# Kernel optimization log

Hardware: AMD Instinct MI355X
Metric: run time of the kernel (lower is better)

The kernel has to match this reference:

```python
import jax, jax.numpy as jnp
import numpy as np

EMBED_DIM = 768
NUM_HEADS = 12
HEAD_DIM = EMBED_DIM // NUM_HEADS


def setup_inputs() -> dict:
    key = jax.random.key(0)
    ks = jax.random.split(key, 12)
    B, T, D, Hp, Wp = 4, 32, EMBED_DIM, 16, 16
    h = jax.random.normal(ks[0], (B, T, D, Hp, Wp), dtype=jnp.float32)
    u_enc = jax.random.uniform(ks[1], (B, T, D, Hp, Wp), dtype=jnp.float32)
    lam = jax.random.uniform(ks[2], (B, T, 1, Hp, Wp), dtype=jnp.float32)
    s = 1.0 / np.sqrt(D)
    Wq = jax.random.normal(ks[3], (D, D), dtype=jnp.float32) * s
    bq = jnp.zeros((D,), dtype=jnp.float32)
    Wk = jax.random.normal(ks[4], (D, D), dtype=jnp.float32) * s
    bk = jnp.zeros((D,), dtype=jnp.float32)
    Wv = jax.random.normal(ks[5], (D, D), dtype=jnp.float32) * s
    bv = jnp.zeros((D,), dtype=jnp.float32)
    Wo = jax.random.normal(ks[6], (D, D), dtype=jnp.float32) * s
    bo = jnp.zeros((D,), dtype=jnp.float32)
    return {"h": h, "u_enc": u_enc, "lam": lam,
            "Wq": Wq, "bq": bq, "Wk": Wk, "bk": bk,
            "Wv": Wv, "bv": bv, "Wo": Wo, "bo": bo}


def reference(h, u_enc, lam, Wq, bq, Wk, bk, Wv, bv, Wo, bo):
    B, T, D, Hp, Wp = h.shape
    S = Hp * Wp
    NH, HD = NUM_HEADS, HEAD_DIM
    # (B,T,D,Hp,Wp) -> (B*S, T, D)
    h_seq = jnp.transpose(h, (0, 3, 4, 1, 2)).reshape(B * S, T, D)
    u_seq = jnp.transpose(u_enc, (0, 3, 4, 1, 2)).reshape(B * S, T, D)
    lam_seq = jnp.transpose(lam, (0, 3, 4, 1, 2)).reshape(B * S, T)
    # projections (nn.Linear: x @ W.T + b)
    Q = (h_seq @ Wq.T + bq).reshape(B * S, T, NH, HD).transpose(0, 2, 1, 3)
    K = (h_seq @ Wk.T + bk).reshape(B * S, T, NH, HD).transpose(0, 2, 1, 3)
    V = (h_seq @ Wv.T + bv).reshape(B * S, T, NH, HD).transpose(0, 2, 1, 3)
    scores = jnp.einsum('bhqd,bhkd->bhqk', Q, K) / jnp.sqrt(jnp.float32(HD))
    # key-dependent uncertainty penalty: lam_j * mean_d(u_j)
    u_pen = lam_seq * u_seq.mean(axis=-1)  # (B*S, T)
    scores = scores - u_pen[:, None, None, :]
    attn = jax.nn.softmax(scores, axis=-1)  # dropout: eval mode (identity)
    out = jnp.einsum('bhqk,bhkd->bhqd', attn, V)
    out = out.transpose(0, 2, 1, 3).reshape(B * S, T, D)
    out = out @ Wo.T + bo
    return jnp.transpose(out.reshape(B, Hp, Wp, T, D), (0, 3, 4, 1, 2))
```

## Files before the change

kernel.cpp:

```cpp
#include <hip/hip_runtime.h>

typedef float   f32x4 __attribute__((ext_vector_type(4)));
typedef _Float16 f16x8 __attribute__((ext_vector_type(8)));

#define DEV static __device__ __forceinline__

#define BB 4
#define TT 32
#define DD 768
#define SS 256
#define NHD 12
#define HD 64
#define NSEQ  (BB*SS)
#define MTOK  (NSEQ*TT)

DEV void async_copy16(const _Float16* g, _Float16* l) {
  __builtin_amdgcn_global_load_lds(
      (const __attribute__((address_space(1))) unsigned int*)g,
      (__attribute__((address_space(3))) unsigned int*)l,
      16, 0, 0);
}

DEV int swz_chunk(int r, int kc) {
  return r * 4 + (kc ^ (r & 3) ^ ((r >> 2) & 3));
}

__global__ __launch_bounds__(256) void k_transpose_h(const float* __restrict__ h,
                                                     _Float16* __restrict__ A) {
  __shared__ _Float16 Tl[256 * 65];
  const int slab = blockIdx.x;
  const int d0   = blockIdx.y * 64;
  const int t    = threadIdx.x;
  const float4* hv = (const float4*)(h + (slab * DD + d0) * SS);
  #pragma unroll
  for (int i = 0; i < 16; ++i) {
    int dd = i * 4 + (t >> 6);
    int s4 = (t & 63) * 4;
    float4 v = hv[dd * 64 + (t & 63)];
    Tl[(s4 + 0) * 65 + dd] = (_Float16)v.x;
    Tl[(s4 + 1) * 65 + dd] = (_Float16)v.y;
    Tl[(s4 + 2) * 65 + dd] = (_Float16)v.z;
    Tl[(s4 + 3) * 65 + dd] = (_Float16)v.w;
  }
  __syncthreads();
  #pragma unroll
  for (int p = 0; p < 8; ++p) {
    int s  = p * 32 + (t >> 3);
    int dd = (t & 7) * 8;
    f16x8 val;
    #pragma unroll
    for (int j = 0; j < 8; ++j) val[j] = Tl[s * 65 + dd + j];
    *(f16x8*)(A + (slab * SS + s) * DD + d0 + dd) = val;
  }
}

__global__ __launch_bounds__(256) void k_convert_w(const float* __restrict__ Wq,
                                                   const float* __restrict__ Wk,
                                                   const float* __restrict__ Wv,
                                                   const float* __restrict__ Wo,
                                                   _Float16* __restrict__ WQKV,
                                                   _Float16* __restrict__ WoH) {
  int idx = blockIdx.x * 256 + threadIdx.x;
  int row = idx / 96;
  int c8  = (idx % 96) * 8;
  const float* src; _Float16* dst;
  if (row < 768)       { src = Wq + row * 768;          dst = WQKV + row * 768; }
  else if (row < 1536) { src = Wk + (row - 768) * 768;  dst = WQKV + row * 768; }
  else if (row < 2304) { src = Wv + (row - 1536) * 768; dst = WQKV + row * 768; }
  else                 { src = Wo + (row - 2304) * 768; dst = WoH  + (row - 2304) * 768; }
  float4 v0 = *(const float4*)(src + c8);
  float4 v1 = *(const float4*)(src + c8 + 4);
  f16x8 o;
  o[0]=(_Float16)v0.x; o[1]=(_Float16)v0.y; o[2]=(_Float16)v0.z; o[3]=(_Float16)v0.w;
  o[4]=(_Float16)v1.x; o[5]=(_Float16)v1.y; o[6]=(_Float16)v1.z; o[7]=(_Float16)v1.w;
  *(f16x8*)(dst + c8) = o;
}

__global__ __launch_bounds__(256) void k_upen(const float* __restrict__ u,
                                              const float* __restrict__ lam,
                                              float* __restrict__ upen) {
  int slab = blockIdx.x >> 2;
  int q    = blockIdx.x & 3;
  int s    = threadIdx.x;
  const float* base = u + (slab * DD + q * 192) * SS + s;
  float sum = 0.f;
  for (int d = 0; d < 192; ++d) sum += base[d * SS];
  int b = slab >> 5, tt = slab & 31;
  float l = lam[slab * SS + s];
  atomicAdd(&upen[(b * SS + s) * TT + tt], sum * l * (1.0f / 768.0f));
}

__global__ __launch_bounds__(256, 2) void k_gemm_qkv(const _Float16* __restrict__ A,
                                                     const _Float16* __restrict__ Bw,
                                                     const float* __restrict__ bq,
                                                     const float* __restrict__ bk,
                                                     const float* __restrict__ bv,
                                                     _Float16* __restrict__ Qp,
                                                     _Float16* __restrict__ Kp,
                                                     _Float16* __restrict__ Vp) {
  __shared__ _Float16 As[128 * 32];
  __shared__ _Float16 Bs[256 * 32];
  const int mt = blockIdx.x & 255, nt = blockIdx.x >> 8;
  const int m0 = mt * 128, n0 = nt * 256;
  const int tid = threadIdx.x, w = tid >> 6, lane = tid & 63;
  const int wr = (w >> 1) * 64, wcc = (w & 1) * 128;
  f32x4 acc[4][8] = {};
  for (int it = 0; it < 24; ++it) {
    const int k0 = it * 32;
    __syncthreads();
    #pragma unroll
    for (int i = 0; i < 2; ++i) {
      int c = tid + 256 * i;
      int row = c >> 2;
      int coff = ((c & 3) ^ (row & 3) ^ ((row >> 2) & 3)) * 8;
      _Float16* ldsA = (_Float16*)((char*)As + (w * 1024 + i * 4096 + lane * 16));
      async_copy16(A + (m0 + row) * DD + k0 + coff, ldsA);
    }
    #pragma unroll
    for (int i = 0; i < 4; ++i) {
      int c = tid + 256 * i;
      int row = c >> 2;
      int coff = ((c & 3) ^ (row & 3) ^ ((row >> 2) & 3)) * 8;
      _Float16* ldsB = (_Float16*)((char*)Bs + (w * 1024 + i * 4096 + lane * 16));
      async_copy16(Bw + (n0 + row) * DD + k0 + coff, ldsB);
    }
    __syncthreads();
    f16x8 af[4], bf[8];
    #pragma unroll
    for (int mi = 0; mi < 4; ++mi)
      af[mi] = *(const f16x8*)&As[swz_chunk(wr + mi * 16 + (lane & 15), lane >> 4) * 8];
    #pragma unroll
    for (int ni = 0; ni < 8; ++ni)
      bf[ni] = *(const f16x8*)&Bs[swz_chunk(wcc + ni * 16 + (lane & 15), lane >> 4) * 8];
    #pragma unroll
    for (int mi = 0; mi < 4; ++mi)
      #pragma unroll
      for (int ni = 0; ni < 8; ++ni)
        acc[mi][ni] = __builtin_amdgcn_mfma_f32_16x16x32_f16(af[mi], bf[ni], acc[mi][ni], 0, 0, 0);
  }
  const int sel = nt / 3;
  const float scale = (sel == 0) ? 0.125f : 1.0f;
  const float* bias = (sel == 0) ? bq : ((sel == 1) ? bk : bv);
  _Float16* dst = (sel == 0) ? Qp : ((sel == 1) ? Kp : Vp);
  const int slab = mt >> 1, s0 = (mt & 1) * 128;
  const int b = slab >> 5, t = slab & 31;
  #pragma unroll
  for (int ni = 0; ni < 8; ++ni) {
    int n768 = nt * 256 - sel * 768 + wcc + ni * 16 + (lane & 15);
    int head = n768 >> 6, hd = n768 & 63;
    float bs = bias[n768];
    long hb = (long)head * 2048 + t * 64 + hd;
    #pragma unroll
    for (int mi = 0; mi < 4; ++mi) {
      f32x4 v = acc[mi][ni];
      #pragma unroll
      for (int r = 0; r < 4; ++r) {
        int s = s0 + wr + mi * 16 + (lane >> 4) * 4 + r;
        long seq = b * 256 + s;
        dst[seq * 24576 + hb] = (_Float16)((v[r] + bs) * scale);
      }
    }
  }
}

__global__ __launch_bounds__(256) void k_attn(const _Float16* __restrict__ Qp,
                                              const _Float16* __restrict__ Kp,
                                              const _Float16* __restrict__ Vp,
                                              const float* __restrict__ upen,
                                              _Float16* __restrict__ O) {
  __shared__ _Float16 lds[4][32 * 66 + 32 * 40];
  const int w = threadIdx.x >> 6, lane = threadIdx.x & 63;
  const int seq = blockIdx.x / 3, hg = blockIdx.x % 3;
  const int head = hg * 4 + w;
  const int b = seq >> 8, s = seq & 255;
  _Float16* Vs = &lds[w][0];
  _Float16* Ps = &lds[w][32 * 66];
  const long base = (long)(seq * NHD + head) * 2048;
  const _Float16* Qb = Qp + base;
  const _Float16* Kb = Kp + base;
  const _Float16* Vb = Vp + base;

  {
    int t = lane & 31, hh = (lane >> 5) * 32;
    f16x8 vc[4];
    #pragma unroll
    for (int c = 0; c < 4; ++c) vc[c] = *(const f16x8*)(Vb + t * 64 + hh + c * 8);
    #pragma unroll
    for (int c = 0; c < 4; ++c)
      #pragma unroll
      for (int p = 0; p < 4; ++p) {
        union { _Float16 h[2]; unsigned u; } pk;
        pk.h[0] = vc[c][2 * p]; pk.h[1] = vc[c][2 * p + 1];
        *(unsigned*)&Vs[t * 66 + hh + c * 8 + 2 * p] = pk.u;
      }
  }
  f16x8 qf[2][2], kf[2][2];
  #pragma unroll
  for (int i = 0; i < 2; ++i)
    #pragma unroll
    for (int ks = 0; ks < 2; ++ks) {
      int off = (i * 16 + (lane & 15)) * 64 + ks * 32 + (lane >> 4) * 8;
      qf[i][ks] = *(const f16x8*)(Qb + off);
      kf[i][ks] = *(const f16x8*)(Kb + off);
    }
  f32x4 sc[2][2] = {};
  #pragma unroll
  for (int mq = 0; mq < 2; ++mq)
    #pragma unroll
    for (int nk = 0; nk < 2; ++nk)
      #pragma unroll
      for (int ks = 0; ks < 2; ++ks)
        sc[mq][nk] = __builtin_amdgcn_mfma_f32_16x16x32_f16(qf[mq][ks], kf[nk][ks], sc[mq][nk], 0, 0, 0);

  const float up0 = upen[seq * TT + (lane & 15)];
  const float up1 = upen[seq * TT + 16 + (lane & 15)];

  #pragma unroll
  for (int mq = 0; mq < 2; ++mq) {
    #pragma unroll
    for (int r = 0; r < 4; ++r) {
      float s0 = sc[mq][0][r] - up0;
      float s1 = sc[mq][1][r] - up1;
      float mx = fmaxf(s0, s1);
      #pragma unroll
      for (int off = 1; off < 16; off <<= 1) mx = fmaxf(mx, __shfl_xor(mx, off, 64));
      float e0 = __expf(s0 - mx), e1 = __expf(s1 - mx);
      float sum = e0 + e1;
      #pragma unroll
      for (int off = 1; off < 16; off <<= 1) sum += __shfl_xor(sum, off, 64);
      float inv = 1.0f / sum;
      int row = mq * 16 + (lane >> 4) * 4 + r;
      Ps[row * 40 + (lane & 15)]      = (_Float16)(e0 * inv);
      Ps[row * 40 + 16 + (lane & 15)] = (_Float16)(e1 * inv);
    }
  }
  f16x8 pf[2];
  #pragma unroll
  for (int mq = 0; mq < 2; ++mq)
    pf[mq] = *(const f16x8*)(Ps + (mq * 16 + (lane & 15)) * 40 + (lane >> 4) * 8);
  f32x4 oacc[2][4] = {};
  #pragma unroll
  for (int nh = 0; nh < 4; ++nh) {
    int hd = nh * 16 + (lane & 15);
    f16x8 vf;
    #pragma unroll
    for (int j = 0; j < 8; ++j) vf[j] = Vs[((lane >> 4) * 8 + j) * 66 + hd];
    #pragma unroll
    for (int mq = 0; mq < 2; ++mq)
      oacc[mq][nh] = __builtin_amdgcn_mfma_f32_16x16x32_f16(pf[mq], vf, oacc[mq][nh], 0, 0, 0);
  }
  #pragma unroll
  for (int mq = 0; mq < 2; ++mq)
    #pragma unroll
    for (int nh = 0; nh < 4; ++nh) {
      int hd = nh * 16 + (lane & 15);
      #pragma unroll
      for (int r = 0; r < 4; ++r) {
        int t = mq * 16 + (lane >> 4) * 4 + r;
        O[((long)((b << 5) + t) * SS + s) * DD + head * HD + hd] = (_Float16)oacc[mq][nh][r];
      }
    }
}

__global__ __launch_bounds__(256, 2) void k_gemm_out(const _Float16* __restrict__ Wn,
                                                     const _Float16* __restrict__ O,
                                                     const float* __restrict__ bo,
                                                     float* __restrict__ out) {
  __shared__ _Float16 As[128 * 32];
  __shared__ _Float16 Bs[256 * 32];
  const int ct = blockIdx.x & 127, rt = blockIdx.x >> 7;
  const int R0 = rt * 128, C0 = ct * 256;
  const int tid = threadIdx.x, w = tid >> 6, lane = tid & 63;
  const int wr = (w >> 1) * 64, wcc = (w & 1) * 128;
  f32x4 acc[4][8] = {};
  for (int it = 0; it < 24; ++it) {
    const int k0 = it * 32;
    __syncthreads();
    #pragma unroll
    for (int i = 0; i < 2; ++i) {
      int c = tid + 256 * i;
      int row = c >> 2;
      int coff = ((c & 3) ^ (row & 3) ^ ((row >> 2) & 3)) * 8;
      _Float16* ldsA = (_Float16*)((char*)As + (w * 1024 + i * 4096 + lane * 16));
      async_copy16(Wn + (R0 + row) * DD + k0 + coff, ldsA);
    }
    #pragma unroll
    for (int i = 0; i < 4; ++i) {
      int c = tid + 256 * i;
      int row = c >> 2;
      int coff = ((c & 3) ^ (row & 3) ^ ((row >> 2) & 3)) * 8;
      _Float16* ldsB = (_Float16*)((char*)Bs + (w * 1024 + i * 4096 + lane * 16));
      async_copy16(O + (C0 + row) * DD + k0 + coff, ldsB);
    }
    __syncthreads();
    f16x8 af[4], bf[8];
    #pragma unroll
    for (int ri = 0; ri < 4; ++ri)
      af[ri] = *(const f16x8*)&As[swz_chunk(wr + ri * 16 + (lane & 15), lane >> 4) * 8];
    #pragma unroll
    for (int ci = 0; ci < 8; ++ci)
      bf[ci] = *(const f16x8*)&Bs[swz_chunk(wcc + ci * 16 + (lane & 15), lane >> 4) * 8];
    #pragma unroll
    for (int ri = 0; ri < 4; ++ri)
      #pragma unroll
      for (int ci = 0; ci < 8; ++ci)
        acc[ri][ci] = __builtin_amdgcn_mfma_f32_16x16x32_f16(af[ri], bf[ci], acc[ri][ci], 0, 0, 0);
  }
  const int slab = ct;
  #pragma unroll
  for (int ri = 0; ri < 4; ++ri) {
    #pragma unroll
    for (int ci = 0; ci < 8; ++ci) {
      int s = wcc + ci * 16 + (lane & 15);
      f32x4 v = acc[ri][ci];
      #pragma unroll
      for (int r = 0; r < 4; ++r) {
        int R = R0 + wr + ri * 16 + (lane >> 4) * 4 + r;
        out[((long)slab * DD + R) * SS + s] = v[r] + bo[R];
      }
    }
  }
}

extern "C" void kernel_launch(void* const* d_in, const int* in_sizes, int n_in,
                              void* d_out, int out_size, void* d_ws, size_t ws_size,
                              hipStream_t stream) {
  const float* h   = (const float*)d_in[0];
  const float* u   = (const float*)d_in[1];
  const float* lam = (const float*)d_in[2];
  const float* Wq  = (const float*)d_in[3];
  const float* bq  = (const float*)d_in[4];
  const float* Wk  = (const float*)d_in[5];
  const float* bk  = (const float*)d_in[6];
  const float* Wv  = (const float*)d_in[7];
  const float* bv  = (const float*)d_in[8];
  const float* Wo  = (const float*)d_in[9];
  const float* bo  = (const float*)d_in[10];
  float* out = (float*)d_out;

  char* ws = (char*)d_ws;
  _Float16* Abuf = (_Float16*)(ws);
  _Float16* WQKV = (_Float16*)(ws + 50331648);
  _Float16* WoH  = (_Float16*)(ws + 53870592);
  float*    upen = (float*)   (ws + 55050240);
  _Float16* Qp   = (_Float16*)(ws + 55181312);
  _Float16* Kp   = (_Float16*)(ws + 105512960);
  _Float16* Vp   = (_Float16*)(ws + 155844608);

  hipMemsetAsync(upen, 0, 32768 * sizeof(float), stream);
  k_transpose_h<<<dim3(128, 12), 256, 0, stream>>>(h, Abuf);
  k_convert_w<<<1152, 256, 0, stream>>>(Wq, Wk, Wv, Wo, WQKV, WoH);
  k_upen<<<512, 256, 0, stream>>>(u, lam, upen);
  k_gemm_qkv<<<256 * 9, 256, 0, stream>>>(Abuf, WQKV, bq, bk, bv, Qp, Kp, Vp);
  k_attn<<<1024 * 3, 256, 0, stream>>>(Qp, Kp, Vp, upen, Abuf);
  k_gemm_out<<<128 * 6, 256, 0, stream>>>(WoH, Abuf, bo, out);
}
```

Measured before the change: 533.7 us.

## Fuse prep kernels and switch GEMMs to single-wave direct-load tiles

Merges the h transpose, weight conversion and uncertainty-penalty kernels into one launch to cut launch overhead. Both GEMMs become 64-thread single-wavefront blocks with 64x128 tiles that load MFMA fragments straight from global memory, dropping LDS staging and barriers. Block indices are grouped so neighbouring blocks share A rows for L2 reuse. The trade-off is less data reuse per block and more global traffic through the cache, in exchange for no synchronisation and more blocks in flight.

Result: slower. 746.5 us (+39.9%).

```diff
diff --git a/kernel.cpp b/kernel.cpp
--- a/kernel.cpp
+++ b/kernel.cpp
@@ -14,150 +14,124 @@
 #define NSEQ  (BB*SS)
 #define MTOK  (NSEQ*TT)
 
-DEV void async_copy16(const _Float16* g, _Float16* l) {
-  __builtin_amdgcn_global_load_lds(
-      (const __attribute__((address_space(1))) unsigned int*)g,
-      (__attribute__((address_space(3))) unsigned int*)l,
-      16, 0, 0);
-}
-
-DEV int swz_chunk(int r, int kc) {
-  return r * 4 + (kc ^ (r & 3) ^ ((r >> 2) & 3));
-}
-
-__global__ __launch_bounds__(256) void k_transpose_h(const float* __restrict__ h,
-                                                     _Float16* __restrict__ A) {
+__global__ __launch_bounds__(256) void k_prep(const float* __restrict__ h,
+                                              const float* __restrict__ u,
+                                              const float* __restrict__ lam,
+                                              const float* __restrict__ Wq,
+                                              const float* __restrict__ Wk,
+                                              const float* __restrict__ Wv,
+                                              const float* __restrict__ Wo,
+                                              _Float16* __restrict__ A,
+                                              _Float16* __restrict__ WQKV,
+                                              _Float16* __restrict__ WoH,
+                                              float* __restrict__ upen) {
   __shared__ _Float16 Tl[256 * 65];
-  const int slab = blockIdx.x;
-  const int d0   = blockIdx.y * 64;
-  const int t    = threadIdx.x;
-  const float4* hv = (const float4*)(h + (slab * DD + d0) * SS);
-  #pragma unroll
-  for (int i = 0; i < 16; ++i) {
-    int dd = i * 4 + (t >> 6);
-    int s4 = (t & 63) * 4;
-    float4 v = hv[dd * 64 + (t & 63)];
-    Tl[(s4 + 0) * 65 + dd] = (_Float16)v.x;
-    Tl[(s4 + 1) * 65 + dd] = (_Float16)v.y;
-    Tl[(s4 + 2) * 65 + dd] = (_Float16)v.z;
-    Tl[(s4 + 3) * 65 + dd] = (_Float16)v.w;
-  }
-  __syncthreads();
-  #pragma unroll
-  for (int p = 0; p < 8; ++p) {
-    int s  = p * 32 + (t >> 3);
-    int dd = (t & 7) * 8;
-    f16x8 val;
-    #pragma unroll
-    for (int j = 0; j < 8; ++j) val[j] = Tl[s * 65 + dd + j];
-    *(f16x8*)(A + (slab * SS + s) * DD + d0 + dd) = val;
-  }
-}
-
-__global__ __launch_bounds__(256) void k_convert_w(const float* __restrict__ Wq,
-                                                   const float* __restrict__ Wk,
-                                                   const float* __restrict__ Wv,
-                                                   const float* __restrict__ Wo,
-                                                   _Float16* __restrict__ WQKV,
-                                                   _Float16* __restrict__ WoH) {
-  int idx = blockIdx.x * 256 + threadIdx.x;
-  int row = idx / 96;
-  int c8  = (idx % 96) * 8;
-  const float* src; _Float16* dst;
-  if (row < 768)       { src = Wq + row * 768;          dst = WQKV + row * 768; }
-  else if (row < 1536) { src = Wk + (row - 768) * 768;  dst = WQKV + row * 768; }
-  else if (row < 2304) { src = Wv + (row - 1536) * 768; dst = WQKV + row * 768; }
-  else                 { src = Wo + (row - 2304) * 768; dst = WoH  + (row - 2304) * 768; }
-  float4 v0 = *(const float4*)(src + c8);
-  float4 v1 = *(const float4*)(src + c8 + 4);
-  f16x8 o;
-  o[0]=(_Float16)v0.x; o[1]=(_Float16)v0.y; o[2]=(_Float16)v0.z; o[3]=(_Float16)v0.w;
-  o[4]=(_Float16)v1.x; o[5]=(_Float16)v1.y; o[6]=(_Float16)v1.z; o[7]=(_Float16)v1.w;
-  *(f16x8*)(dst + c8) = o;
-}
-
-__global__ __launch_bounds__(256) void k_upen(const float* __restrict__ u,
-                                              const float* __restrict__ lam,
-                                              float* __restrict__ upen) {
-  int slab = blockIdx.x >> 2;
-  int q    = blockIdx.x & 3;
-  int s    = threadIdx.x;
-  const float* base = u + (slab * DD + q * 192) * SS + s;
-  float sum = 0.f;
-  for (int d = 0; d < 192; ++d) sum += base[d * SS];
-  int b = slab >> 5, tt = slab & 31;
-  float l = lam[slab * SS + s];
-  atomicAdd(&upen[(b * SS + s) * TT + tt], sum * l * (1.0f / 768.0f));
-}
-
-__global__ __launch_bounds__(256, 2) void k_gemm_qkv(const _Float16* __restrict__ A,
-                                                     const _Float16* __restrict__ Bw,
-                                                     const float* __restrict__ bq,
-                                                     const float* __restrict__ bk,
-                                                     const float* __restrict__ bv,
-                                                     _Float16* __restrict__ Qp,
-                                                     _Float16* __restrict__ Kp,
-                                                     _Float16* __restrict__ Vp) {
-  __shared__ _Float16 As[128 * 32];
-  __shared__ _Float16 Bs[256 * 32];
-  const int mt = blockIdx.x & 255, nt = blockIdx.x >> 8;
-  const int m0 = mt * 128, n0 = nt * 256;
-  const int tid = threadIdx.x, w = tid >> 6, lane = tid & 63;
-  const int wr = (w >> 1) * 64, wcc = (w & 1) * 128;
+  const int blk = blockIdx.x;
+  const int t = threadIdx.x;
+  if (blk < 1536) {
+    const int slab = blk & 127;
+    const int d0   = (blk >> 7) * 64;
+    const float4* hv = (const float4*)(h + (slab * DD + d0) * SS);
+    #pragma unroll
+    for (int i = 0; i < 16; ++i) {
+      int dd = i * 4 + (t >> 6);
+      int s4 = (t & 63) * 4;
+      float4 v = hv[dd * 64 + (t & 63)];
+      Tl[(s4 + 0) * 65 + dd] = (_Float16)v.x;
+      Tl[(s4 + 1) * 65 + dd] = (_Float16)v.y;
+      Tl[(s4 + 2) * 65 + dd] = (_Float16)v.z;
+      Tl[(s4 + 3) * 65 + dd] = (_Float16)v.w;
+    }
+    __syncthreads();
+    #pragma unroll
+    for (int p = 0; p < 8; ++p) {
+      int s  = p * 32 + (t >> 3);
+      int dd = (t & 7) * 8;
+      f16x8 val;
+      #pragma unroll
+      for (int j = 0; j < 8; ++j) val[j] = Tl[s * 65 + dd + j];
+      *(f16x8*)(A + (slab * SS + s) * DD + d0 + dd) = val;
+    }
+  } else if (blk < 1536 + 1152) {
+    int idx = (blk - 1536) * 256 + t;
+    int row = idx / 96;
+    int c8  = (idx % 96) * 8;
+    const float* src; _Float16* dst;
+    if (row < 768)       { src = Wq + row * 768;          dst = WQKV + row * 768; }
+    else if (row < 1536) { src = Wk + (row - 768) * 768;  dst = WQKV + row * 768; }
+    else if (row < 2304) { src = Wv + (row - 1536) * 768; dst = WQKV + row * 768; }
+    else                 { src = Wo + (row - 2304) * 768; dst = WoH  + (row - 2304) * 768; }
+    float4 v0 = *(const float4*)(src + c8);
+    float4 v1 = *(const float4*)(src + c8 + 4);
+    f16x8 o;
+    o[0]=(_Float16)v0.x; o[1]=(_Float16)v0.y; o[2]=(_Float16)v0.z; o[3]=(_Float16)v0.w;
+    o[4]=(_Float16)v1.x; o[5]=(_Float16)v1.y; o[6]=(_Float16)v1.z; o[7]=(_Float16)v1.w;
+    *(f16x8*)(dst + c8) = o;
+  } else {
+    int ublk = blk - 2688;
+    int slab = ublk >> 2;
+    int q    = ublk & 3;
+    int s    = t;
+    const float* base = u + (slab * DD + q * 192) * SS + s;
+    float sum = 0.f;
+    for (int d = 0; d < 192; ++d) sum += base[d * SS];
+    int b = slab >> 5, tt = slab & 31;
+    float l = lam[slab * SS + s];
+    atomicAdd(&upen[(b * SS + s) * TT + tt], sum * l * (1.0f / 768.0f));
+  }
+}
+
+__global__ __launch_bounds__(64, 2) void k_gemm_qkv(const _Float16* __restrict__ A,
+                                                    const _Float16* __restrict__ Bw,
+                                                    const float* __restrict__ bq,
+                                                    const float* __restrict__ bk,
+                                                    const float* __restrict__ bv,
+                                                    _Float16* __restrict__ Qp,
+                                                    _Float16* __restrict__ Kp,
+                                                    _Float16* __restrict__ Vp) {
+  const int bidx = blockIdx.x;
+  const int mtg = bidx / 144, rem = bidx % 144;
+  const int nt = rem >> 3, mt = mtg * 8 + (rem & 7);
+  const int m0 = mt * 64, n0 = nt * 128;
+  const int lane = threadIdx.x;
+  const int lr = lane & 15, lk = (lane >> 4) * 8;
+  const _Float16* ap = A  + (long)(m0 + lr) * DD + lk;
+  const _Float16* bp = Bw + (long)(n0 + lr) * DD + lk;
   f32x4 acc[4][8] = {};
+  #pragma unroll
   for (int it = 0; it < 24; ++it) {
-    const int k0 = it * 32;
-    __syncthreads();
-    #pragma unroll
-    for (int i = 0; i < 2; ++i) {
-      int c = tid + 256 * i;
-      int row = c >> 2;
-      int coff = ((c & 3) ^ (row & 3) ^ ((row >> 2) & 3)) * 8;
-      _Float16* ldsA = (_Float16*)((char*)As + (w * 1024 + i * 4096 + lane * 16));
-      async_copy16(A + (m0 + row) * DD + k0 + coff, ldsA);
-    }
-    #pragma unroll
-    for (int i = 0; i < 4; ++i) {
-      int c = tid + 256 * i;
-      int row = c >> 2;
-      int coff = ((c & 3) ^ (row & 3) ^ ((row >> 2) & 3)) * 8;
-      _Float16* ldsB = (_Float16*)((char*)Bs + (w * 1024 + i * 4096 + lane * 16));
-      async_copy16(Bw + (n0 + row) * DD + k0 + coff, ldsB);
-    }
-    __syncthreads();
+    const int ko = it * 32;
     f16x8 af[4], bf[8];
     #pragma unroll
-    for (int mi = 0; mi < 4; ++mi)
-      af[mi] = *(const f16x8*)&As[swz_chunk(wr + mi * 16 + (lane & 15), lane >> 4) * 8];
-    #pragma unroll
-    for (int ni = 0; ni < 8; ++ni)
-      bf[ni] = *(const f16x8*)&Bs[swz_chunk(wcc + ni * 16 + (lane & 15), lane >> 4) * 8];
+    for (int mi = 0; mi < 4; ++mi) af[mi] = *(const f16x8*)(ap + mi * (16 * DD) + ko);
+    #pragma unroll
+    for (int ni = 0; ni < 8; ++ni) bf[ni] = *(const f16x8*)(bp + ni * (16 * DD) + ko);
     #pragma unroll
     for (int mi = 0; mi < 4; ++mi)
       #pragma unroll
       for (int ni = 0; ni < 8; ++ni)
         acc[mi][ni] = __builtin_amdgcn_mfma_f32_16x16x32_f16(af[mi], bf[ni], acc[mi][ni], 0, 0, 0);
   }
-  const int sel = nt / 3;
+  const int sel = nt / 6;
   const float scale = (sel == 0) ? 0.125f : 1.0f;
   const float* bias = (sel == 0) ? bq : ((sel == 1) ? bk : bv);
   _Float16* dst = (sel == 0) ? Qp : ((sel == 1) ? Kp : Vp);
-  const int slab = mt >> 1, s0 = (mt & 1) * 128;
-  const int b = slab >> 5, t = slab & 31;
+  const int slab = mt >> 2, s0 = (mt & 3) * 64;
+  const int bb = slab >> 5, tt = slab & 31;
   #pragma unroll
   for (int ni = 0; ni < 8; ++ni) {
-    int n768 = nt * 256 - sel * 768 + wcc + ni * 16 + (lane & 15);
+    int n768 = n0 - sel * 768 + ni * 16 + lr;
     int head = n768 >> 6, hd = n768 & 63;
-    float bs = bias[n768];
-    long hb = (long)head * 2048 + t * 64 + hd;
+    float bsv = bias[n768];
+    long hb = (long)head * 2048 + tt * 64 + hd;
     #pragma unroll
     for (int mi = 0; mi < 4; ++mi) {
       f32x4 v = acc[mi][ni];
       #pragma unroll
       for (int r = 0; r < 4; ++r) {
-        int s = s0 + wr + mi * 16 + (lane >> 4) * 4 + r;
-        long seq = b * 256 + s;
-        dst[seq * 24576 + hb] = (_Float16)((v[r] + bs) * scale);
+        int s = s0 + mi * 16 + (lane >> 4) * 4 + r;
+        long seq = bb * 256 + s;
+        dst[seq * 24576 + hb] = (_Float16)((v[r] + bsv) * scale);
       }
     }
   }
@@ -262,60 +236,43 @@
     }
 }
 
-__global__ __launch_bounds__(256, 2) void k_gemm_out(const _Float16* __restrict__ Wn,
-                                                     const _Float16* __restrict__ O,
-                                                     const float* __restrict__ bo,
-                                                     float* __restrict__ out) {
-  __shared__ _Float16 As[128 * 32];
-  __shared__ _Float16 Bs[256 * 32];
-  const int ct = blockIdx.x & 127, rt = blockIdx.x >> 7;
-  const int R0 = rt * 128, C0 = ct * 256;
-  const int tid = threadIdx.x, w = tid >> 6, lane = tid & 63;
-  const int wr = (w >> 1) * 64, wcc = (w & 1) * 128;
+__global__ __launch_bounds__(64, 2) void k_gemm_out(const _Float16* __restrict__ Wn,
+                                                    const _Float16* __restrict__ O,
+                                                    const float* __restrict__ bo,
+                                                    float* __restrict__ out) {
+  const int bidx = blockIdx.x;
+  const int ctg = bidx / 96, rem = bidx % 96;
+  const int rt = rem >> 3, ct = ctg * 8 + (rem & 7);
+  const int R0 = rt * 64, C0 = ct * 128;
+  const int lane = threadIdx.x;
+  const int lr = lane & 15, lk = (lane >> 4) * 8;
+  const _Float16* ap = Wn + (long)(R0 + lr) * DD + lk;
+  const _Float16* bp = O  + (long)(C0 + lr) * DD + lk;
   f32x4 acc[4][8] = {};
+  #pragma unroll
   for (int it = 0; it < 24; ++it) {
-    const int k0 = it * 32;
-    __syncthreads();
-    #pragma unroll
-    for (int i = 0; i < 2; ++i) {
-      int c = tid + 256 * i;
-      int row = c >> 2;
-      int coff = ((c & 3) ^ (row & 3) ^ ((row >> 2) & 3)) * 8;
-      _Float16* ldsA = (_Float16*)((char*)As + (w * 1024 + i * 4096 + lane * 16));
-      async_copy16(Wn + (R0 + row) * DD + k0 + coff, ldsA);
-    }
-    #pragma unroll
-    for (int i = 0; i < 4; ++i) {
-      int c = tid + 256 * i;
-      int row = c >> 2;
-      int coff = ((c & 3) ^ (row & 3) ^ ((row >> 2) & 3)) * 8;
-      _Float16* ldsB = (_Float16*)((char*)Bs + (w * 1024 + i * 4096 + lane * 16));
-      async_copy16(O + (C0 + row) * DD + k0 + coff, ldsB);
-    }
-    __syncthreads();
+    const int ko = it * 32;
     f16x8 af[4], bf[8];
     #pragma unroll
-    for (int ri = 0; ri < 4; ++ri)
-      af[ri] = *(const f16x8*)&As[swz_chunk(wr + ri * 16 + (lane & 15), lane >> 4) * 8];
-    #pragma unroll
-    for (int ci = 0; ci < 8; ++ci)
-      bf[ci] = *(const f16x8*)&Bs[swz_chunk(wcc + ci * 16 + (lane & 15), lane >> 4) * 8];
+    for (int ri = 0; ri < 4; ++ri) af[ri] = *(const f16x8*)(ap + ri * (16 * DD) + ko);
+    #pragma unroll
+    for (int ci = 0; ci < 8; ++ci) bf[ci] = *(const f16x8*)(bp + ci * (16 * DD) + ko);
     #pragma unroll
     for (int ri = 0; ri < 4; ++ri)
       #pragma unroll
       for (int ci = 0; ci < 8; ++ci)
         acc[ri][ci] = __builtin_amdgcn_mfma_f32_16x16x32_f16(af[ri], bf[ci], acc[ri][ci], 0, 0, 0);
   }
-  const int slab = ct;
+  const int slab = C0 >> 8, sbase = C0 & 255;
   #pragma unroll
   for (int ri = 0; ri < 4; ++ri) {
     #pragma unroll
     for (int ci = 0; ci < 8; ++ci) {
-      int s = wcc + ci * 16 + (lane & 15);
+      int s = sbase + ci * 16 + lr;
       f32x4 v = acc[ri][ci];
       #pragma unroll
       for (int r = 0; r < 4; ++r) {
-        int R = R0 + wr + ri * 16 + (lane >> 4) * 4 + r;
+        int R = R0 + ri * 16 + (lane >> 4) * 4 + r;
         out[((long)slab * DD + R) * SS + s] = v[r] + bo[R];
       }
     }
@@ -348,10 +305,8 @@
   _Float16* Vp   = (_Float16*)(ws + 155844608);
 
   hipMemsetAsync(upen, 0, 32768 * sizeof(float), stream);
-  k_transpose_h<<<dim3(128, 12), 256, 0, stream>>>(h, Abuf);
-  k_convert_w<<<1152, 256, 0, stream>>>(Wq, Wk, Wv, Wo, WQKV, WoH);
-  k_upen<<<512, 256, 0, stream>>>(u, lam, upen);
-  k_gemm_qkv<<<256 * 9, 256, 0, stream>>>(Abuf, WQKV, bq, bk, bv, Qp, Kp, Vp);
+  k_prep<<<3200, 256, 0, stream>>>(h, u, lam, Wq, Wk, Wv, Wo, Abuf, WQKV, WoH, upen);
+  k_gemm_qkv<<<9216, 64, 0, stream>>>(Abuf, WQKV, bq, bk, bv, Qp, Kp, Vp);
   k_attn<<<1024 * 3, 256, 0, stream>>>(Qp, Kp, Vp, upen, Abuf);
-  k_gemm_out<<<128 * 6, 256, 0, stream>>>(WoH, Abuf, bo, out);
-}
+  k_gemm_out<<<3072, 64, 0, stream>>>(WoH, Abuf, bo, out);
+}
```
